# Performance work log

Hardware: AMD Instinct MI355X
Metric: run time of the kernel (lower is better)

Reference implementation:

```python
import jax, jax.numpy as jnp
import numpy as np

MIN_DELAY = 60
MAX_DELAY = 420
TAU = 0.0          # module's self.tau (min magnitude for resonant_activation)
TEMPERATURE = 1.0  # forward() default gumbel-softmax temperature


def setup_inputs() -> dict:
    key = jax.random.key(0)
    k1, k2, k3, k4 = jax.random.split(key, 4)
    B, T = 128, 8192
    excitation = jax.random.normal(k1, (B, 1, T), dtype=jnp.float32)
    u = jax.random.uniform(k2, (MAX_DELAY - MIN_DELAY,), dtype=jnp.float32,
                           minval=1e-6, maxval=1.0 - 1e-6)
    gumbel_noise = -jnp.log(-jnp.log(u))  # standard Gumbel samples
    delay_param = jax.random.normal(k3, (MAX_DELAY - MIN_DELAY,), dtype=jnp.float32)
    feedback_gain = jnp.ones((1,), dtype=jnp.float32)
    reflection_coeffs = jax.random.normal(k4, (2,), dtype=jnp.float32)
    return {"excitation": excitation, "gumbel_noise": gumbel_noise,
            "delay_param": delay_param, "feedback_gain": feedback_gain,
            "reflection_coeffs": reflection_coeffs}


def _resonant_activation(x, min_magnitude):
    sign = jnp.sign(x)
    magnitude = jnp.abs(jnp.tanh(x))
    return sign * (min_magnitude + (1.0 - min_magnitude) * magnitude)


def _build_coeffs(gumbel_noise, delay_param, feedback_gain, reflection_coeffs):
    # gumbel_softmax(tau=TEMPERATURE, hard=True) with straight-through estimator
    logits = (delay_param + gumbel_noise) / TEMPERATURE
    soft = jax.nn.softmax(logits)
    hard = jax.nn.one_hot(jnp.argmax(soft), soft.shape[0], dtype=soft.dtype)
    one_hot = jax.lax.stop_gradient(hard - soft) + soft
    shifted = jnp.roll(one_hot, 1)
    # low_pass_bias=False -> tanh, then resonant_activation (applies tanh again, as in source)
    rc = jnp.tanh(reflection_coeffs)
    k1 = _resonant_activation(rc[0], TAU)
    k2 = _resonant_activation(rc[1], TAU)
    a1 = k1 * (1.0 - k2)
    a2 = jnp.clip(k2, -0.999, 0.999)
    a1_bound = 0.999 - jnp.abs(a2)
    a1 = jnp.clip(a1, -a1_bound, a1_bound)
    g = jax.nn.sigmoid(feedback_gain[0]) ** 0.45
    a1 = a1 * g
    a2 = a2 * g
    tail = one_hot * a1 + shifted * a2               # [max_delay - min_delay]
    coeffs = jnp.concatenate([jnp.zeros((MIN_DELAY,), tail.dtype), tail])  # [max_delay]
    return coeffs


def _sample_wise_lpc(x, coeffs):
    # All-pole IIR: y[t] = x[t] - sum_{i=0}^{D-1} coeffs[i] * y[t-1-i]
    B, T = x.shape
    D = coeffs.shape[0]
    buf0 = jnp.zeros((B, D), x.dtype)  # buf[:, i] = y[t-1-i]

    def step(buf, x_t):
        y_t = x_t - buf @ coeffs                              # [B]
        buf = jnp.concatenate([y_t[:, None], buf[:, :-1]], 1)  # shift delay line
        return buf, y_t

    _, ys = jax.lax.scan(step, buf0, x.T)  # ys: [T, B]
    return ys.T


def reference(excitation, gumbel_noise, delay_param, feedback_gain, reflection_coeffs):
    coeffs = _build_coeffs(gumbel_noise, delay_param, feedback_gain, reflection_coeffs)
    x = excitation[:, 0, :]                 # [B, T]
    y = _sample_wise_lpc(x, coeffs)         # [B, T]
    return y[:, None, :]                    # [B, 1, T]
```

## Files before the change

kernel.cpp:

```cpp
#include <hip/hip_runtime.h>
#include <cmath>

#define T_LEN 8192
#define B_ROWS 128
#define ND 360
#define MIN_DELAY_C 60
#define BLOCK 256
#define NCH (T_LEN / BLOCK)


template<int NT>
__device__ __forceinline__ void fir_pass(const float* __restrict__ src,
                                         float* __restrict__ dst,
                                         const float* __restrict__ sc,
                                         const int* __restrict__ sl,
                                         int maxlag, int tid)
{
    float c[NT]; int l[NT];
#pragma unroll
    for (int j = 0; j < NT; ++j) { c[j] = sc[j]; l[j] = sl[j]; }

    int kStart = (maxlag + BLOCK - 1) / BLOCK;
    if (kStart > NCH) kStart = NCH;
    const int kB = NCH - ((NCH - kStart) & ~3);

    for (int k = 0; k < kB; ++k) {
        const int t = tid + k * BLOCK;
        float r[NT + 1];
        r[0] = src[t];
#pragma unroll
        for (int j = 0; j < NT; ++j) {
            int s = t - l[j];
            r[j + 1] = (s >= 0) ? src[s] : 0.0f;
        }
        float acc = r[0];
#pragma unroll
        for (int j = 0; j < NT; ++j) acc += c[j] * r[j + 1];
        dst[t] = acc;
    }
    for (int k = kB; k < NCH; k += 4) {
        float r[4][NT + 1];
#pragma unroll
        for (int u = 0; u < 4; ++u) {
            const int t = tid + (k + u) * BLOCK;
            r[u][0] = src[t];
#pragma unroll
            for (int j = 0; j < NT; ++j) r[u][j + 1] = src[t - l[j]];
        }
#pragma unroll
        for (int u = 0; u < 4; ++u) {
            const int t = tid + (k + u) * BLOCK;
            float acc = r[u][0];
#pragma unroll
            for (int j = 0; j < NT; ++j) acc += c[j] * r[u][j + 1];
            dst[t] = acc;
        }
    }
}

__global__ __launch_bounds__(BLOCK) void ks_resonator_kernel(
    const float* __restrict__ excitation,
    const float* __restrict__ gumbel,
    const float* __restrict__ delay_param,
    const float* __restrict__ feedback_gain,
    const float* __restrict__ refl,
    float* __restrict__ out)
{
    __shared__ float bufA[T_LEN];
    __shared__ float bufB[T_LEN];
    __shared__ float s_c1[2], s_c2[3], s_c4[5], s_c8[9];
    __shared__ int   s_l1[2], s_l2[3], s_l4[5], s_l8[9];
    __shared__ int   s_dA, s_dB;

    const int tid = threadIdx.x;
    const int row = blockIdx.x;

    if (tid < 192) {
        const float4* __restrict__ x4 = (const float4*)(excitation + (size_t)row * T_LEN);
        float4* a4 = (float4*)bufA;
        for (int i = tid; i < T_LEN / 4; i += 192) a4[i] = x4[i];
    } else {
        const int lane = tid - 192;
        float v = -INFINITY; int idx = 0;
        for (int i = lane; i < ND; i += 64) {
            float w = delay_param[i] + gumbel[i];
            if (w > v) { v = w; idx = i; }
        }
#pragma unroll
        for (int off = 32; off > 0; off >>= 1) {
            float v2 = __shfl_xor(v, off);
            int   i2 = __shfl_xor(idx, off);
            if (v2 > v || (v2 == v && i2 < idx)) { v = v2; idx = i2; }
        }
        if (lane == 0) {
            const int p = idx;
            float k1 = tanhf(tanhf(refl[0]));
            float k2 = tanhf(tanhf(refl[1]));
            float a1 = k1 * (1.0f - k2);
            float a2 = fminf(fmaxf(k2, -0.999f), 0.999f);
            float bound = 0.999f - fabsf(a2);
            a1 = fminf(fmaxf(a1, -bound), bound);
            float fg = feedback_gain[0];
            float g = powf(1.0f / (1.0f + expf(-fg)), 0.45f);
            a1 *= g; a2 *= g;
            const int p2 = (p + 1) % ND;
            const int dA = MIN_DELAY_C + p + 1;
            const int dB = MIN_DELAY_C + p2 + 1;

            float p1[9], q2[9];
            p1[0] = 1.0f; q2[0] = 1.0f;
            for (int i = 1; i < 9; ++i) { p1[i] = p1[i-1] * a1; q2[i] = q2[i-1] * a2; }
            const float C2[3] = {1.f, 2.f, 1.f};
            const float C4[5] = {1.f, 4.f, 6.f, 4.f, 1.f};
            const float C8[9] = {1.f, 8.f, 28.f, 56.f, 70.f, 56.f, 28.f, 8.f, 1.f};
            s_c1[0] = -a1; s_l1[0] = dA;
            s_c1[1] = -a2; s_l1[1] = dB;
            for (int i = 0; i < 3; ++i) { s_c2[i] = C2[i] * p1[i] * q2[2-i]; s_l2[i] = i*dA + (2-i)*dB; }
            for (int i = 0; i < 5; ++i) { s_c4[i] = C4[i] * p1[i] * q2[4-i]; s_l4[i] = i*dA + (4-i)*dB; }
            for (int i = 0; i < 9; ++i) { s_c8[i] = C8[i] * p1[i] * q2[8-i]; s_l8[i] = i*dA + (8-i)*dB; }
            s_dA = dA; s_dB = dB;
        }
    }
    __syncthreads();

    const int dA = s_dA, dB = s_dB;
    const int dmax = (dA > dB) ? dA : dB;

    fir_pass<2>(bufA, bufB, s_c1, s_l1, dmax, tid);
    __syncthreads();

    fir_pass<3>(bufB, bufA, s_c2, s_l2, 2 * dmax, tid);
    __syncthreads();

    fir_pass<5>(bufA, bufB, s_c4, s_l4, 4 * dmax, tid);
    __syncthreads();

    {
        float c[9]; int l[9];
#pragma unroll
        for (int j = 0; j < 9; ++j) { c[j] = s_c8[j]; l[j] = s_l8[j]; }
        const int dmin = (dA < dB) ? dA : dB;
        const int W  = 8 * dmin;
        const int L8 = 8 * dmax;
        for (int pos = 0; pos < T_LEN; pos += W) {
            int end = pos + W; if (end > T_LEN) end = T_LEN;
            if (pos >= L8) {
                int j = pos + tid;
                for (; j + BLOCK < end; j += 2 * BLOCK) {
                    float r0[10], r1[10];
                    r0[0] = bufB[j]; r1[0] = bufB[j + BLOCK];
#pragma unroll
                    for (int k = 0; k < 9; ++k) {
                        r0[k + 1] = bufB[j - l[k]];
                        r1[k + 1] = bufB[j + BLOCK - l[k]];
                    }
                    float a0 = r0[0], a1v = r1[0];
#pragma unroll
                    for (int k = 0; k < 9; ++k) { a0 += c[k] * r0[k + 1]; a1v += c[k] * r1[k + 1]; }
                    bufB[j] = a0; bufB[j + BLOCK] = a1v;
                }
                if (j < end) {
                    float r[10]; r[0] = bufB[j];
#pragma unroll
                    for (int k = 0; k < 9; ++k) r[k + 1] = bufB[j - l[k]];
                    float a0 = r[0];
#pragma unroll
                    for (int k = 0; k < 9; ++k) a0 += c[k] * r[k + 1];
                    bufB[j] = a0;
                }
            } else {
                for (int j = pos + tid; j < end; j += BLOCK) {
                    float r[10]; r[0] = bufB[j];
#pragma unroll
                    for (int k = 0; k < 9; ++k) {
                        int s = j - l[k];
                        r[k + 1] = (s >= 0) ? bufB[s] : 0.0f;
                    }
                    float a0 = r[0];
#pragma unroll
                    for (int k = 0; k < 9; ++k) a0 += c[k] * r[k + 1];
                    bufB[j] = a0;
                }
            }
            __syncthreads();
        }
    }

    float4* __restrict__ o4 = (float4*)(out + (size_t)row * T_LEN);
    const float4* b4 = (const float4*)bufB;
    for (int i = tid; i < T_LEN / 4; i += BLOCK) o4[i] = b4[i];
}

extern "C" void kernel_launch(void* const* d_in, const int* in_sizes, int n_in,
                              void* d_out, int out_size, void* d_ws, size_t ws_size,
                              hipStream_t stream) {
    const float* excitation    = (const float*)d_in[0];
    const float* gumbel        = (const float*)d_in[1];
    const float* delay_param   = (const float*)d_in[2];
    const float* feedback_gain = (const float*)d_in[3];
    const float* refl          = (const float*)d_in[4];
    float* out = (float*)d_out;

    ks_resonator_kernel<<<B_ROWS, BLOCK, 0, stream>>>(
        excitation, gumbel, delay_param, feedback_gain, refl, out);
}
```

Before: 78.05 us.

## Use 1024-thread blocks with float4-grouped FIR passes and branchless masking

```diff
diff --git a/kernel.cpp b/kernel.cpp
--- a/kernel.cpp
+++ b/kernel.cpp
@@ -5,57 +5,37 @@
 #define B_ROWS 128
 #define ND 360
 #define MIN_DELAY_C 60
-#define BLOCK 256
-#define NCH (T_LEN / BLOCK)
+#define BLOCK 1024
+#define GSTRIDE (4 * BLOCK)
 
 
-template<int NT>
-__device__ __forceinline__ void fir_pass(const float* __restrict__ src,
-                                         float* __restrict__ dst,
-                                         const float* __restrict__ sc,
-                                         const int* __restrict__ sl,
-                                         int maxlag, int tid)
+template<int NT, bool MASK>
+__device__ __forceinline__ void fir_group(const float* __restrict__ src,
+                                          float* __restrict__ dst, int t0,
+                                          const float* __restrict__ c,
+                                          const int* __restrict__ l)
 {
-    float c[NT]; int l[NT];
+    const float4 x = *(const float4*)&src[t0];
+    float r[NT][4];
 #pragma unroll
-    for (int j = 0; j < NT; ++j) { c[j] = sc[j]; l[j] = sl[j]; }
-
-    int kStart = (maxlag + BLOCK - 1) / BLOCK;
-    if (kStart > NCH) kStart = NCH;
-    const int kB = NCH - ((NCH - kStart) & ~3);
-
-    for (int k = 0; k < kB; ++k) {
-        const int t = tid + k * BLOCK;
-        float r[NT + 1];
-        r[0] = src[t];
+    for (int j = 0; j < NT; ++j) {
 #pragma unroll
-        for (int j = 0; j < NT; ++j) {
-            int s = t - l[j];
-            r[j + 1] = (s >= 0) ? src[s] : 0.0f;
-        }
-        float acc = r[0];
-#pragma unroll
-        for (int j = 0; j < NT; ++j) acc += c[j] * r[j + 1];
-        dst[t] = acc;
-    }
-    for (int k = kB; k < NCH; k += 4) {
-        float r[4][NT + 1];
-#pragma unroll
-        for (int u = 0; u < 4; ++u) {
-            const int t = tid + (k + u) * BLOCK;
-            r[u][0] = src[t];
-#pragma unroll
-            for (int j = 0; j < NT; ++j) r[u][j + 1] = src[t - l[j]];
-        }
-#pragma unroll
-        for (int u = 0; u < 4; ++u) {
-            const int t = tid + (k + u) * BLOCK;
-            float acc = r[u][0];
-#pragma unroll
-            for (int j = 0; j < NT; ++j) acc += c[j] * r[u][j + 1];
-            dst[t] = acc;
+        for (int e = 0; e < 4; ++e) {
+            const int s = t0 + e - l[j];
+            if (MASK) {
+                const float v = src[(s >= 0) ? s : 0];
+                r[j][e] = (s >= 0) ? v : 0.0f;
+            } else {
+                r[j][e] = src[s];
+            }
         }
     }
+    float acc[4] = {x.x, x.y, x.z, x.w};
+#pragma unroll
+    for (int j = 0; j < NT; ++j)
+#pragma unroll
+        for (int e = 0; e < 4; ++e) acc[e] += c[j] * r[j][e];
+    *(float4*)&dst[t0] = make_float4(acc[0], acc[1], acc[2], acc[3]);
 }
 
 __global__ __launch_bounds__(BLOCK) void ks_resonator_kernel(
@@ -66,8 +46,8 @@
     const float* __restrict__ refl,
     float* __restrict__ out)
 {
-    __shared__ float bufA[T_LEN];
-    __shared__ float bufB[T_LEN];
+    __shared__ __align__(16) float bufA[T_LEN];
+    __shared__ __align__(16) float bufB[T_LEN];
     __shared__ float s_c1[2], s_c2[3], s_c4[5], s_c8[9];
     __shared__ int   s_l1[2], s_l2[3], s_l4[5], s_l8[9];
     __shared__ int   s_dA, s_dB;
@@ -75,12 +55,12 @@
     const int tid = threadIdx.x;
     const int row = blockIdx.x;
 
-    if (tid < 192) {
+    if (tid < 960) {
         const float4* __restrict__ x4 = (const float4*)(excitation + (size_t)row * T_LEN);
         float4* a4 = (float4*)bufA;
-        for (int i = tid; i < T_LEN / 4; i += 192) a4[i] = x4[i];
+        for (int i = tid; i < T_LEN / 4; i += 960) a4[i] = x4[i];
     } else {
-        const int lane = tid - 192;
+        const int lane = tid - 960;
         float v = -INFINITY; int idx = 0;
         for (int i = lane; i < ND; i += 64) {
             float w = delay_param[i] + gumbel[i];
@@ -123,64 +103,58 @@
     }
     __syncthreads();
 
-    const int dA = s_dA, dB = s_dB;
-    const int dmax = (dA > dB) ? dA : dB;
+    const int t0 = 4 * tid;
+    const int t1 = t0 + GSTRIDE;
 
-    fir_pass<2>(bufA, bufB, s_c1, s_l1, dmax, tid);
+    {
+        float c[2]; int l[2];
+#pragma unroll
+        for (int j = 0; j < 2; ++j) { c[j] = s_c1[j]; l[j] = s_l1[j]; }
+        fir_group<2, true >(bufA, bufB, t0, c, l);
+        fir_group<2, false>(bufA, bufB, t1, c, l);
+    }
     __syncthreads();
 
-    fir_pass<3>(bufB, bufA, s_c2, s_l2, 2 * dmax, tid);
+    {
+        float c[3]; int l[3];
+#pragma unroll
+        for (int j = 0; j < 3; ++j) { c[j] = s_c2[j]; l[j] = s_l2[j]; }
+        fir_group<3, true >(bufB, bufA, t0, c, l);
+        fir_group<3, false>(bufB, bufA, t1, c, l);
+    }
     __syncthreads();
 
-    fir_pass<5>(bufA, bufB, s_c4, s_l4, 4 * dmax, tid);
+    {
+        float c[5]; int l[5];
+#pragma unroll
+        for (int j = 0; j < 5; ++j) { c[j] = s_c4[j]; l[j] = s_l4[j]; }
+        fir_group<5, true >(bufA, bufB, t0, c, l);
+        fir_group<5, false>(bufA, bufB, t1, c, l);
+    }
     __syncthreads();
 
     {
         float c[9]; int l[9];
 #pragma unroll
         for (int j = 0; j < 9; ++j) { c[j] = s_c8[j]; l[j] = s_l8[j]; }
+        const int dA = s_dA, dB = s_dB;
         const int dmin = (dA < dB) ? dA : dB;
-        const int W  = 8 * dmin;
-        const int L8 = 8 * dmax;
+        const int W = 8 * dmin;
         for (int pos = 0; pos < T_LEN; pos += W) {
             int end = pos + W; if (end > T_LEN) end = T_LEN;
-            if (pos >= L8) {
-                int j = pos + tid;
-                for (; j + BLOCK < end; j += 2 * BLOCK) {
-                    float r0[10], r1[10];
-                    r0[0] = bufB[j]; r1[0] = bufB[j + BLOCK];
+            for (int j = pos + tid; j < end; j += BLOCK) {
+                float r[10];
+                r[0] = bufB[j];
 #pragma unroll
-                    for (int k = 0; k < 9; ++k) {
-                        r0[k + 1] = bufB[j - l[k]];
-                        r1[k + 1] = bufB[j + BLOCK - l[k]];
-                    }
-                    float a0 = r0[0], a1v = r1[0];
+                for (int k = 0; k < 9; ++k) {
+                    const int s = j - l[k];
+                    const float v = bufB[(s >= 0) ? s : 0];
+                    r[k + 1] = (s >= 0) ? v : 0.0f;
+                }
+                float acc = r[0];
 #pragma unroll
-                    for (int k = 0; k < 9; ++k) { a0 += c[k] * r0[k + 1]; a1v += c[k] * r1[k + 1]; }
-                    bufB[j] = a0; bufB[j + BLOCK] = a1v;
-                }
-                if (j < end) {
-                    float r[10]; r[0] = bufB[j];
-#pragma unroll
-                    for (int k = 0; k < 9; ++k) r[k + 1] = bufB[j - l[k]];
-                    float a0 = r[0];
-#pragma unroll
-                    for (int k = 0; k < 9; ++k) a0 += c[k] * r[k + 1];
-                    bufB[j] = a0;
-                }
-            } else {
-                for (int j = pos + tid; j < end; j += BLOCK) {
-                    float r[10]; r[0] = bufB[j];
-#pragma unroll
-                    for (int k = 0; k < 9; ++k) {
-                        int s = j - l[k];
-                        r[k + 1] = (s >= 0) ? bufB[s] : 0.0f;
-                    }
-                    float a0 = r[0];
-#pragma unroll
-                    for (int k = 0; k < 9; ++k) a0 += c[k] * r[k + 1];
-                    bufB[j] = a0;
-                }
+                for (int k = 0; k < 9; ++k) acc += c[k] * r[k + 1];
+                bufB[j] = acc;
             }
             __syncthreads();
         }
```

After: 74.48 us. 1.05x faster.
